# Performance work log

Hardware: AMD Instinct MI355X
Metric: run time of the kernel (lower is better)

Reference implementation:

```python
import jax, jax.numpy as jnp
import numpy as np

B, IN, E, H, MO, OUT, K = 32768, 512, 8, 128, 256, 2, 2


def setup_inputs() -> dict:
    key = jax.random.key(0)
    ks = jax.random.split(key, 9)
    g = lambda k, shape, fan: (jax.random.normal(k, shape, jnp.float32) / np.sqrt(fan)).astype(jnp.float32)
    return {
        "num_prop": jax.random.normal(ks[0], (B, IN), jnp.float32),
        "cat_prop": jax.random.normal(ks[1], (B, 3), jnp.float32),
        "w_gate": g(ks[2], (IN, E), IN),
        "W1": g(ks[3], (E, IN, H), IN),
        "b1": jnp.zeros((E, H), jnp.float32),
        "W2": g(ks[4], (E, H, MO), H),
        "b2": jnp.zeros((E, MO), jnp.float32),
        "Wout": g(ks[5], (MO, OUT), MO),
        "bout": jnp.zeros((OUT,), jnp.float32),
    }


def _cv_squared(v):
    # torch.var is unbiased (ddof=1); eps = 1e-10
    return jnp.var(v, ddof=1) / (jnp.mean(v) ** 2 + 1e-10)


def reference(num_prop, cat_prop, w_gate, W1, b1, W2, b2, Wout, bout):
    b = num_prop.shape[0]
    x = num_prop  # eval mode: dropout is identity, gating noise disabled
    # --- top-k gating ---
    logits = x @ w_gate                                   # [B, E]
    top_vals, top_idx = jax.lax.top_k(logits, K)          # [B, K]
    gate_vals = jax.nn.softmax(top_vals, axis=-1)         # softmax over top-k logits
    gates = jnp.zeros_like(logits).at[jnp.arange(b)[:, None], top_idx].add(gate_vals)  # [B, E]
    # --- load-balancing loss ---
    importance = gates.sum(axis=0)                        # [E]
    load = (gates > 0).astype(jnp.float32).sum(axis=0)    # [E]
    loss = (_cv_squared(importance) + _cv_squared(load)) * 1e-2
    # --- experts (dense-equivalent: gates zero out non-selected experts) ---
    h = jax.nn.relu(jnp.einsum('bi,eih->beh', x, W1) + b1)          # [B, E, H]
    eo = jax.nn.softmax(jnp.einsum('beh,ehm->bem', h, W2) + b2, axis=-1)  # [B, E, MO]
    y = jnp.einsum('be,bem->bm', gates, eo)               # [B, MO]
    # --- output head ---
    out = y @ Wout + bout                                 # [B, OUT]
    return out, loss
```

## Files before the change

### kernel.cpp

```cpp
#include <hip/hip_runtime.h>

#define BN 32768
#define IN 512
#define NE 8
#define NH 128
#define MO 256

typedef const __attribute__((address_space(1))) unsigned int gu32;
typedef __attribute__((address_space(3))) unsigned int lu32;
typedef __attribute__((ext_vector_type(8))) short bf16x8;
typedef __attribute__((ext_vector_type(4))) float f32x4;

__device__ __forceinline__ void cp16(const float* g, float* l) {
    __builtin_amdgcn_global_load_lds((gu32*)g, (lu32*)l, 16, 0, 0);
}

__device__ __forceinline__ unsigned short f2bf(float f) {
    unsigned int u = __float_as_uint(f);
    u = (u + 0x7fffu + ((u >> 16) & 1u)) >> 16;
    return (unsigned short)u;
}
__device__ __forceinline__ float bf2f(unsigned short h) {
    return __uint_as_float((unsigned int)h << 16);
}

__global__ __launch_bounds__(256) void gatep_kernel(
    const float* __restrict__ x, const float* __restrict__ wg,
    const float* __restrict__ W1, const float* __restrict__ W2,
    float* __restrict__ W1F, float* __restrict__ W2F,
    int* __restrict__ gcount, int* __restrict__ gload, float* __restrict__ gimp,
    int* __restrict__ idx_list, float* __restrict__ gate_list,
    float* __restrict__ out, const float* __restrict__ bout)
{
    __shared__ __align__(16) char wb[32768];
    __shared__ int counts_s[NE];
    __shared__ int load_s[NE];
    __shared__ float imp_s[NE];
    __shared__ int base_s[NE];
    __shared__ int rec_e[128];
    __shared__ int rec_p[128];
    __shared__ float rec_g[128];

    int tid = threadIdx.x;
    int bx = blockIdx.x;

    if (bx >= 512) {
        char* pb = wb;
        int t = tid, b = bx - 512;
        if (b < 64) {
            int e = b >> 3, kt = b & 7;
            const float* src = W1 + ((size_t)e * IN + kt * 64) * NH;
            #pragma unroll
            for (int p = 0; p < 8; ++p) {
                int li = p * 256 + t;
                float4 q = *(const float4*)(src + li * 4);
                int kl = li >> 5, n0 = (li & 31) * 4;
                int ks = kl >> 5, g = (kl >> 3) & 3, kb = (kl & 7) * 2;
                float vv[4] = {q.x, q.y, q.z, q.w};
                #pragma unroll
                for (int j = 0; j < 4; ++j) {
                    int n = n0 + j;
                    int off = (((ks * 8 + (n >> 4)) * 64) + (n & 15) + 16 * g) * 16 + kb;
                    unsigned short hh = f2bf(vv[j]);
                    unsigned short hl = f2bf(vv[j] - bf2f(hh));
                    *(unsigned short*)(pb + off) = hh;
                    *(unsigned short*)(pb + 16384 + off) = hl;
                }
            }
            __syncthreads();
            float* dst = W1F + (size_t)b * 8192;
            #pragma unroll
            for (int p = 0; p < 8; ++p) {
                int li = p * 256 + t;
                *(int4*)(dst + li * 4) = *(const int4*)(pb + li * 16);
            }
        } else {
            int bi = b - 64;
            int e = bi >> 2, kt = bi & 3;
            const float* src = W2 + ((size_t)e * NH + kt * 32) * MO;
            #pragma unroll
            for (int p = 0; p < 8; ++p) {
                int li = p * 256 + t;
                float4 q = *(const float4*)(src + li * 4);
                int kl = li >> 6, n0 = (li & 63) * 4;
                int g = kl >> 3, kb = (kl & 7) * 2;
                float vv[4] = {q.x, q.y, q.z, q.w};
                #pragma unroll
                for (int j = 0; j < 4; ++j) {
                    int n = n0 + j;
                    int off = ((n >> 4) * 64 + (n & 15) + 16 * g) * 16 + kb;
                    unsigned short hh = f2bf(vv[j]);
                    unsigned short hl = f2bf(vv[j] - bf2f(hh));
                    *(unsigned short*)(pb + off) = hh;
                    *(unsigned short*)(pb + 16384 + off) = hl;
                }
            }
            __syncthreads();
            float* dst = W2F + (size_t)bi * 8192;
            #pragma unroll
            for (int p = 0; p < 8; ++p) {
                int li = p * 256 + t;
                *(int4*)(dst + li * 4) = *(const int4*)(pb + li * 16);
            }
        }
        return;
    }

    if (tid < NE) { counts_s[tid] = 0; load_s[tid] = 0; imp_s[tid] = 0.f; }
    if (tid < 128) {
        int row = bx * 64 + (tid >> 1);
        out[row * 2 + (tid & 1)] = bout[tid & 1];
    }
    for (int idx = tid; idx < 1024; idx += 256) {
        int ks = idx >> 6, ls = idx & 63;
        int col = ls & 15;
        int kb = 32 * ks + 8 * (ls >> 4);
        unsigned int ph[4], pl[4];
        #pragma unroll
        for (int j = 0; j < 4; ++j) {
            float v0 = (col < 8) ? wg[(kb + 2 * j) * NE + col] : 0.f;
            float v1 = (col < 8) ? wg[(kb + 2 * j + 1) * NE + col] : 0.f;
            unsigned short h0 = f2bf(v0), h1 = f2bf(v1);
            unsigned short l0 = f2bf(v0 - bf2f(h0)), l1 = f2bf(v1 - bf2f(h1));
            ph[j] = (unsigned int)h0 | ((unsigned int)h1 << 16);
            pl[j] = (unsigned int)l0 | ((unsigned int)l1 << 16);
        }
        *(int4*)(wb + ks * 1024 + ls * 16) = make_int4(ph[0], ph[1], ph[2], ph[3]);
        *(int4*)(wb + 16384 + ks * 1024 + ls * 16) = make_int4(pl[0], pl[1], pl[2], pl[3]);
    }
    __syncthreads();

    int w = tid >> 6, l = tid & 63;
    int e = l & 15;
    int rowA = bx * 64 + w * 16 + e;
    const float* px = x + (size_t)rowA * IN + 8 * (l >> 4);

    f32x4 acc = {};
    #pragma unroll
    for (int ks = 0; ks < 16; ++ks) {
        float4 qa = *(const float4*)(px + 32 * ks);
        float4 qb = *(const float4*)(px + 32 * ks + 4);
        float v[8] = {qa.x, qa.y, qa.z, qa.w, qb.x, qb.y, qb.z, qb.w};
        bf16x8 ah, al;
        #pragma unroll
        for (int i = 0; i < 8; ++i) {
            unsigned short h = f2bf(v[i]);
            ah[i] = (short)h;
            al[i] = (short)f2bf(v[i] - bf2f(h));
        }
        bf16x8 bh = *(const bf16x8*)(wb + ks * 1024 + l * 16);
        bf16x8 bl = *(const bf16x8*)(wb + 16384 + ks * 1024 + l * 16);
        acc = __builtin_amdgcn_mfma_f32_16x16x32_bf16(ah, bh, acc, 0, 0, 0);
        acc = __builtin_amdgcn_mfma_f32_16x16x32_bf16(ah, bl, acc, 0, 0, 0);
        acc = __builtin_amdgcn_mfma_f32_16x16x32_bf16(al, bh, acc, 0, 0, 0);
    }

    #pragma unroll
    for (int reg = 0; reg < 4; ++reg) {
        int rloc = w * 16 + 4 * (l >> 4) + reg;
        int row = bx * 64 + rloc;
        float lv = (e < 8) ? acc[reg] : -1e30f;

        float v0 = lv; int e0 = e;
        #pragma unroll
        for (int m = 1; m < 8; m <<= 1) {
            float vo = __shfl_xor(v0, m, 64);
            int eo = __shfl_xor(e0, m, 64);
            if (vo > v0 || (vo == v0 && eo < e0)) { v0 = vo; e0 = eo; }
        }
        float v1 = (e == e0 || e >= 8) ? -1e30f : lv; int e1 = e;
        #pragma unroll
        for (int m = 1; m < 8; m <<= 1) {
            float vo = __shfl_xor(v1, m, 64);
            int eo = __shfl_xor(e1, m, 64);
            if (vo > v1 || (vo == v1 && eo < e1)) { v1 = vo; e1 = eo; }
        }
        float v2 = (e == e0 || e == e1 || e >= 8) ? -1e30f : lv;
        #pragma unroll
        for (int m = 1; m < 8; m <<= 1) v2 = fmaxf(v2, __shfl_xor(v2, m, 64));

        double dv0 = v0, dv1 = v1;
        int f0 = e0, f1 = e1;
        if (e < 8 && v1 - v2 < 2e-4f) {
            const float* xr = x + (size_t)row * IN;
            double d0 = 0, d1 = 0, d2 = 0, d3 = 0;
            for (int k = 0; k < IN; k += 4) {
                float4 xv = *(const float4*)(xr + k);
                d0 = fma((double)xv.x, (double)wg[(k    ) * NE + e], d0);
                d1 = fma((double)xv.y, (double)wg[(k + 1) * NE + e], d1);
                d2 = fma((double)xv.z, (double)wg[(k + 2) * NE + e], d2);
                d3 = fma((double)xv.w, (double)wg[(k + 3) * NE + e], d3);
            }
            double ad = (d0 + d1) + (d2 + d3);
            double w0 = ad; int g0i = e;
            #pragma unroll
            for (int m = 1; m < 8; m <<= 1) {
                double vo = __shfl_xor(w0, m, 64);
                int eo = __shfl_xor(g0i, m, 64);
                if (vo > w0 || (vo == w0 && eo < g0i)) { w0 = vo; g0i = eo; }
            }
            double w1 = (e == g0i) ? -1.0e300 : ad; int g1i = e;
            #pragma unroll
            for (int m = 1; m < 8; m <<= 1) {
                double vo = __shfl_xor(w1, m, 64);
                int eo = __shfl_xor(g1i, m, 64);
                if (vo > w1 || (vo == w1 && eo < g1i)) { w1 = vo; g1i = eo; }
            }
            dv0 = w0; dv1 = w1; f0 = g0i; f1 = g1i;
        }

        if (e == 0) {
            float t1 = expf((float)(dv1 - dv0));
            float s = 1.f + t1;
            float g0 = 1.f / s;
            float g1 = t1 / s;
            atomicAdd(&imp_s[f0], g0);
            atomicAdd(&imp_s[f1], g1);
            if (g0 > 0.f) atomicAdd(&load_s[f0], 1);
            if (g1 > 0.f) atomicAdd(&load_s[f1], 1);
            int p0 = atomicAdd(&counts_s[f0], 1);
            int p1 = atomicAdd(&counts_s[f1], 1);
            int rl = rloc * 2;
            rec_e[rl] = f0; rec_e[rl + 1] = f1;
            rec_g[rl] = g0; rec_g[rl + 1] = g1;
            rec_p[rl] = p0; rec_p[rl + 1] = p1;
        }
    }
    __syncthreads();
    if (tid < NE) {
        base_s[tid] = atomicAdd(&gcount[tid], counts_s[tid]);
        atomicAdd(&gimp[tid], imp_s[tid]);
        atomicAdd(&gload[tid], load_s[tid]);
    }
    __syncthreads();
    if (tid < 128) {
        int ee = rec_e[tid];
        int pos = base_s[ee] + rec_p[tid];
        int rw = bx * 64 + (tid >> 1);
        idx_list[ee * BN + pos] = rw;
        gate_list[ee * BN + pos] = rec_g[tid];
    }
}

__global__ __launch_bounds__(256, 3) void expert_kernel(
    const float* __restrict__ x,
    const float* __restrict__ b1, const float* __restrict__ b2,
    const float* __restrict__ Wout,
    const float* __restrict__ W1F, const float* __restrict__ W2F,
    const int* __restrict__ gcount,
    const float* __restrict__ gimp, const int* __restrict__ gload,
    const int* __restrict__ idx_list, const float* __restrict__ gate_list,
    float* __restrict__ out)
{
    __shared__ __align__(16) char smx[49152];
    __shared__ float woutS[512];

    int e = blockIdx.y;
    int cnt = gcount[e];
    int row0 = blockIdx.x * 64;
    if (e == 0 && blockIdx.x == 0 && threadIdx.x == 0) {
        float mi = 0.f, ml = 0.f;
        for (int k = 0; k < NE; ++k) { mi += gimp[k]; ml += (float)gload[k]; }
        mi *= 0.125f; ml *= 0.125f;
        float vi = 0.f, vl = 0.f;
        for (int k = 0; k < NE; ++k) {
            float d = gimp[k] - mi;  vi += d * d;
            float d2 = (float)gload[k] - ml; vl += d2 * d2;
        }
        vi *= (1.f / 7.f); vl *= (1.f / 7.f);
        out[BN * 2] = (vi / (mi * mi + 1e-10f) + vl / (ml * ml + 1e-10f)) * 0.01f;
    }
    if (row0 >= cnt) return;
    int t = threadIdx.x;
    int l = t & 63, w = t >> 6;

    woutS[t] = Wout[t];
    woutS[256 + t] = Wout[256 + t];

    int s_r  = t & 15;
    int s_g  = (t >> 4) & 3;
    int s_mf = t >> 6;
    int rloc_s = s_mf * 16 + s_r;
    int sgi = row0 + rloc_s; if (sgi >= cnt) sgi = cnt - 1;
    const float* xrow = x + (size_t)idx_list[e * BN + sgi] * IN;

    const float* W1e = W1F + (size_t)e * 65536;
    const float* W2e = W2F + (size_t)e * 32768;

    f32x4 acc1[8] = {};
    for (int kt = 0; kt < 8; ++kt) {
        {
            const float* gb = W1e + (size_t)kt * 8192;
            float* lb = (float*)(smx + 16384);
            #pragma unroll
            for (int p = 0; p < 8; ++p)
                cp16(gb + (p * 256 + t) * 4, lb + (p * 256 + t) * 4);
        }
        #pragma unroll
        for (int ks = 0; ks < 2; ++ks) {
            int k = kt * 64 + ks * 32 + s_g * 8;
            float4 qa = *(const float4*)(xrow + k);
            float4 qb = *(const float4*)(xrow + k + 4);
            float vv[8] = {qa.x, qa.y, qa.z, qa.w, qb.x, qb.y, qb.z, qb.w};
            unsigned int dh[4], dl[4];
            #pragma unroll
            for (int j = 0; j < 4; ++j) {
                unsigned short h0 = f2bf(vv[2 * j]);
                unsigned short h1 = f2bf(vv[2 * j + 1]);
                unsigned short l0 = f2bf(vv[2 * j] - bf2f(h0));
                unsigned short l1 = f2bf(vv[2 * j + 1] - bf2f(h1));
                dh[j] = (unsigned int)h0 | ((unsigned int)h1 << 16);
                dl[j] = (unsigned int)l0 | ((unsigned int)l1 << 16);
            }
            int slot = ((ks * 4 + s_mf) * 64 + (s_r + 16 * s_g)) * 16;
            *(int4*)(smx + slot) = make_int4(dh[0], dh[1], dh[2], dh[3]);
            *(int4*)(smx + 8192 + slot) = make_int4(dl[0], dl[1], dl[2], dl[3]);
        }
        __syncthreads();
        #pragma unroll
        for (int ks = 0; ks < 2; ++ks) {
            int ao = ((ks * 4 + w) * 64 + l) * 16;
            bf16x8 ah = *(const bf16x8*)(smx + ao);
            bf16x8 al = *(const bf16x8*)(smx + 8192 + ao);
            #pragma unroll
            for (int nf = 0; nf < 8; ++nf) {
                int bo = ((ks * 8 + nf) * 64 + l) * 16;
                bf16x8 bh = *(const bf16x8*)(smx + 16384 + bo);
                bf16x8 bl = *(const bf16x8*)(smx + 32768 + bo);
                acc1[nf] = __builtin_amdgcn_mfma_f32_16x16x32_bf16(ah, bh, acc1[nf], 0, 0, 0);
                acc1[nf] = __builtin_amdgcn_mfma_f32_16x16x32_bf16(ah, bl, acc1[nf], 0, 0, 0);
                acc1[nf] = __builtin_amdgcn_mfma_f32_16x16x32_bf16(al, bh, acc1[nf], 0, 0, 0);
                acc1[nf] = __builtin_amdgcn_mfma_f32_16x16x32_bf16(al, bl, acc1[nf], 0, 0, 0);
            }
        }
        __syncthreads();
    }

    {
        int rlow = 4 * (l >> 4);
        #pragma unroll
        for (int nf = 0; nf < 8; ++nf) {
            int c = nf * 16 + (l & 15);
            float b1v = b1[e * NH + c];
            int kt2c = c >> 5;
            int g2 = (c >> 3) & 3;
            int boff = ((kt2c * 4 + w) * 64) * 16 + (c & 7) * 2;
            #pragma unroll
            for (int rg = 0; rg < 4; ++rg) {
                float v = fmaxf(acc1[nf][rg] + b1v, 0.f);
                unsigned short hh = f2bf(v);
                unsigned short hl = f2bf(v - bf2f(hh));
                int off = boff + ((rlow + rg) + 16 * g2) * 16;
                *(unsigned short*)(smx + off) = hh;
                *(unsigned short*)(smx + 16384 + off) = hl;
            }
        }
    }
    __syncthreads();

    f32x4 acc2[16] = {};
    for (int kt2 = 0; kt2 < 4; ++kt2) {
        int ao = ((kt2 * 4 + w) * 64 + l) * 16;
        bf16x8 ah2 = *(const bf16x8*)(smx + ao);
        bf16x8 al2 = *(const bf16x8*)(smx + 16384 + ao);
        #pragma unroll
        for (int nh2 = 0; nh2 < 2; ++nh2) {
            {
                const float* gh = W2e + kt2 * 8192 + nh2 * 2048;
                const float* gl = W2e + kt2 * 8192 + 4096 + nh2 * 2048;
                float* lb = (float*)(smx + 32768);
                #pragma unroll
                for (int p = 0; p < 2; ++p) {
                    cp16(gh + (p * 256 + t) * 4, lb + (p * 256 + t) * 4);
                    cp16(gl + (p * 256 + t) * 4, lb + 2048 + (p * 256 + t) * 4);
                }
            }
            __syncthreads();
            #pragma unroll
            for (int nf2 = 0; nf2 < 8; ++nf2) {
                int bo = (nf2 * 64 + l) * 16;
                bf16x8 bh = *(const bf16x8*)(smx + 32768 + bo);
                bf16x8 bl = *(const bf16x8*)(smx + 40960 + bo);
                int nf = nh2 * 8 + nf2;
                acc2[nf] = __builtin_amdgcn_mfma_f32_16x16x32_bf16(ah2, bh, acc2[nf], 0, 0, 0);
                acc2[nf] = __builtin_amdgcn_mfma_f32_16x16x32_bf16(ah2, bl, acc2[nf], 0, 0, 0);
                acc2[nf] = __builtin_amdgcn_mfma_f32_16x16x32_bf16(al2, bh, acc2[nf], 0, 0, 0);
                acc2[nf] = __builtin_amdgcn_mfma_f32_16x16x32_bf16(al2, bl, acc2[nf], 0, 0, 0);
            }
            __syncthreads();
        }
    }

    #pragma unroll
    for (int nf = 0; nf < 16; ++nf) {
        float b2v = b2[e * MO + nf * 16 + (l & 15)];
        #pragma unroll
        for (int rg = 0; rg < 4; ++rg) acc2[nf][rg] += b2v;
    }
    #pragma unroll
    for (int rg = 0; rg < 4; ++rg) {
        float m = -1e30f;
        #pragma unroll
        for (int nf = 0; nf < 16; ++nf) m = fmaxf(m, acc2[nf][rg]);
        m = fmaxf(m, __shfl_xor(m, 1, 64));
        m = fmaxf(m, __shfl_xor(m, 2, 64));
        m = fmaxf(m, __shfl_xor(m, 4, 64));
        m = fmaxf(m, __shfl_xor(m, 8, 64));
        float s = 0.f, o0 = 0.f, o1 = 0.f;
        #pragma unroll
        for (int nf = 0; nf < 16; ++nf) {
            float tt = __expf(acc2[nf][rg] - m);
            s += tt;
            float2 wv = *(const float2*)&woutS[2 * (nf * 16 + (l & 15))];
            o0 = fmaf(tt, wv.x, o0);
            o1 = fmaf(tt, wv.y, o1);
        }
        s += __shfl_xor(s, 1, 64); s += __shfl_xor(s, 2, 64);
        s += __shfl_xor(s, 4, 64); s += __shfl_xor(s, 8, 64);
        o0 += __shfl_xor(o0, 1, 64); o0 += __shfl_xor(o0, 2, 64);
        o0 += __shfl_xor(o0, 4, 64); o0 += __shfl_xor(o0, 8, 64);
        o1 += __shfl_xor(o1, 1, 64); o1 += __shfl_xor(o1, 2, 64);
        o1 += __shfl_xor(o1, 4, 64); o1 += __shfl_xor(o1, 8, 64);
        if ((l & 15) == 0) {
            int gi = row0 + w * 16 + 4 * (l >> 4) + rg;
            if (gi < cnt) {
                float g = gate_list[e * BN + gi];
                int brow = idx_list[e * BN + gi];
                float inv = 1.f / s;
                atomicAdd(&out[brow * 2 + 0], g * o0 * inv);
                atomicAdd(&out[brow * 2 + 1], g * o1 * inv);
            }
        }
    }
}

extern "C" void kernel_launch(void* const* d_in, const int* in_sizes, int n_in,
                              void* d_out, int out_size, void* d_ws, size_t ws_size,
                              hipStream_t stream) {
    const float* x    = (const float*)d_in[0];
    const float* wg   = (const float*)d_in[2];
    const float* W1   = (const float*)d_in[3];
    const float* b1   = (const float*)d_in[4];
    const float* W2   = (const float*)d_in[5];
    const float* b2   = (const float*)d_in[6];
    const float* Wout = (const float*)d_in[7];
    const float* bout = (const float*)d_in[8];
    float* out = (float*)d_out;

    char* ws = (char*)d_ws;
    int*   gcount    = (int*)(ws + 0);
    int*   gload     = (int*)(ws + 32);
    float* gimp      = (float*)(ws + 64);
    int*   idx_list  = (int*)(ws + 128);
    float* gate_list = (float*)(ws + 128 + sizeof(int) * NE * BN);
    float* W1F       = (float*)(ws + 128 + 8 * NE * BN);
    float* W2F       = (float*)(ws + 128 + 8 * NE * BN + 64 * 32768);

    hipMemsetAsync(ws, 0, 128, stream);
    gatep_kernel<<<608, 256, 0, stream>>>(x, wg, W1, W2, W1F, W2F,
                                          gcount, gload, gimp,
                                          idx_list, gate_list, out, bout);
    dim3 eg(BN / 64, NE);
    expert_kernel<<<eg, 256, 0, stream>>>(x, b1, b2, Wout, W1F, W2F,
                                          gcount, gimp, gload,
                                          idx_list, gate_list, out);
}
```

Measured before the change: 209.0 us.

## Split expert GEMM wave tiling into 2x2 M/N grid with cross-wave softmax reduction

```diff
diff --git a/kernel.cpp b/kernel.cpp
--- a/kernel.cpp
+++ b/kernel.cpp
@@ -253,7 +253,8 @@
     float* __restrict__ out)
 {
     __shared__ __align__(16) char smx[49152];
-    __shared__ float woutS[512];
+    __shared__ float redm[64][2];
+    __shared__ float red3[64][2][3];
 
     int e = blockIdx.y;
     int cnt = gcount[e];
@@ -273,9 +274,8 @@
     if (row0 >= cnt) return;
     int t = threadIdx.x;
     int l = t & 63, w = t >> 6;
-
-    woutS[t] = Wout[t];
-    woutS[256 + t] = Wout[256 + t];
+    int wm = w & 1;
+    int wn = w >> 1;
 
     int s_r  = t & 15;
     int s_g  = (t >> 4) & 3;
@@ -287,7 +287,7 @@
     const float* W1e = W1F + (size_t)e * 65536;
     const float* W2e = W2F + (size_t)e * 32768;
 
-    f32x4 acc1[8] = {};
+    f32x4 acc1[2][4] = {};
     for (int kt = 0; kt < 8; ++kt) {
         {
             const float* gb = W1e + (size_t)kt * 8192;
@@ -319,18 +319,25 @@
         __syncthreads();
         #pragma unroll
         for (int ks = 0; ks < 2; ++ks) {
-            int ao = ((ks * 4 + w) * 64 + l) * 16;
-            bf16x8 ah = *(const bf16x8*)(smx + ao);
-            bf16x8 al = *(const bf16x8*)(smx + 8192 + ao);
-            #pragma unroll
-            for (int nf = 0; nf < 8; ++nf) {
-                int bo = ((ks * 8 + nf) * 64 + l) * 16;
+            bf16x8 ah[2], al[2];
+            #pragma unroll
+            for (int mf = 0; mf < 2; ++mf) {
+                int ao = ((ks * 4 + wm * 2 + mf) * 64 + l) * 16;
+                ah[mf] = *(const bf16x8*)(smx + ao);
+                al[mf] = *(const bf16x8*)(smx + 8192 + ao);
+            }
+            #pragma unroll
+            for (int nfl = 0; nfl < 4; ++nfl) {
+                int bo = ((ks * 8 + wn * 4 + nfl) * 64 + l) * 16;
                 bf16x8 bh = *(const bf16x8*)(smx + 16384 + bo);
                 bf16x8 bl = *(const bf16x8*)(smx + 32768 + bo);
-                acc1[nf] = __builtin_amdgcn_mfma_f32_16x16x32_bf16(ah, bh, acc1[nf], 0, 0, 0);
-                acc1[nf] = __builtin_amdgcn_mfma_f32_16x16x32_bf16(ah, bl, acc1[nf], 0, 0, 0);
-                acc1[nf] = __builtin_amdgcn_mfma_f32_16x16x32_bf16(al, bh, acc1[nf], 0, 0, 0);
-                acc1[nf] = __builtin_amdgcn_mfma_f32_16x16x32_bf16(al, bl, acc1[nf], 0, 0, 0);
+                #pragma unroll
+                for (int mf = 0; mf < 2; ++mf) {
+                    acc1[mf][nfl] = __builtin_amdgcn_mfma_f32_16x16x32_bf16(ah[mf], bh, acc1[mf][nfl], 0, 0, 0);
+                    acc1[mf][nfl] = __builtin_amdgcn_mfma_f32_16x16x32_bf16(ah[mf], bl, acc1[mf][nfl], 0, 0, 0);
+                    acc1[mf][nfl] = __builtin_amdgcn_mfma_f32_16x16x32_bf16(al[mf], bh, acc1[mf][nfl], 0, 0, 0);
+                    acc1[mf][nfl] = __builtin_amdgcn_mfma_f32_16x16x32_bf16(al[mf], bl, acc1[mf][nfl], 0, 0, 0);
+                }
             }
         }
         __syncthreads();
@@ -339,35 +346,43 @@
     {
         int rlow = 4 * (l >> 4);
         #pragma unroll
-        for (int nf = 0; nf < 8; ++nf) {
-            int c = nf * 16 + (l & 15);
-            float b1v = b1[e * NH + c];
-            int kt2c = c >> 5;
-            int g2 = (c >> 3) & 3;
-            int boff = ((kt2c * 4 + w) * 64) * 16 + (c & 7) * 2;
-            #pragma unroll
-            for (int rg = 0; rg < 4; ++rg) {
-                float v = fmaxf(acc1[nf][rg] + b1v, 0.f);
-                unsigned short hh = f2bf(v);
-                unsigned short hl = f2bf(v - bf2f(hh));
-                int off = boff + ((rlow + rg) + 16 * g2) * 16;
-                *(unsigned short*)(smx + off) = hh;
-                *(unsigned short*)(smx + 16384 + off) = hl;
+        for (int mf = 0; mf < 2; ++mf) {
+            int mf2 = wm * 2 + mf;
+            #pragma unroll
+            for (int nfl = 0; nfl < 4; ++nfl) {
+                int c = wn * 64 + nfl * 16 + (l & 15);
+                float b1v = b1[e * NH + c];
+                int kt2c = c >> 5;
+                int g2 = (c >> 3) & 3;
+                int boff = ((kt2c * 4 + mf2) * 64) * 16 + (c & 7) * 2;
+                #pragma unroll
+                for (int rg = 0; rg < 4; ++rg) {
+                    float v = fmaxf(acc1[mf][nfl][rg] + b1v, 0.f);
+                    unsigned short hh = f2bf(v);
+                    unsigned short hl = f2bf(v - bf2f(hh));
+                    int off = boff + ((rlow + rg) + 16 * g2) * 16;
+                    *(unsigned short*)(smx + off) = hh;
+                    *(unsigned short*)(smx + 16384 + off) = hl;
+                }
             }
         }
     }
     __syncthreads();
 
-    f32x4 acc2[16] = {};
+    f32x4 acc2[2][8] = {};
     for (int kt2 = 0; kt2 < 4; ++kt2) {
-        int ao = ((kt2 * 4 + w) * 64 + l) * 16;
-        bf16x8 ah2 = *(const bf16x8*)(smx + ao);
-        bf16x8 al2 = *(const bf16x8*)(smx + 16384 + ao);
-        #pragma unroll
-        for (int nh2 = 0; nh2 < 2; ++nh2) {
+        bf16x8 ah2[2], al2[2];
+        #pragma unroll
+        for (int mf = 0; mf < 2; ++mf) {
+            int ao = ((kt2 * 4 + wm * 2 + mf) * 64 + l) * 16;
+            ah2[mf] = *(const bf16x8*)(smx + ao);
+            al2[mf] = *(const bf16x8*)(smx + 16384 + ao);
+        }
+        #pragma unroll
+        for (int ch = 0; ch < 2; ++ch) {
             {
-                const float* gh = W2e + kt2 * 8192 + nh2 * 2048;
-                const float* gl = W2e + kt2 * 8192 + 4096 + nh2 * 2048;
+                const float* gh = W2e + kt2 * 8192 + ch * 2048;
+                const float* gl = W2e + kt2 * 8192 + 4096 + ch * 2048;
                 float* lb = (float*)(smx + 32768);
                 #pragma unroll
                 for (int p = 0; p < 2; ++p) {
@@ -377,60 +392,95 @@
             }
             __syncthreads();
             #pragma unroll
-            for (int nf2 = 0; nf2 < 8; ++nf2) {
-                int bo = (nf2 * 64 + l) * 16;
+            for (int nf2 = 0; nf2 < 4; ++nf2) {
+                int bo = ((wn * 4 + nf2) * 64 + l) * 16;
                 bf16x8 bh = *(const bf16x8*)(smx + 32768 + bo);
                 bf16x8 bl = *(const bf16x8*)(smx + 40960 + bo);
-                int nf = nh2 * 8 + nf2;
-                acc2[nf] = __builtin_amdgcn_mfma_f32_16x16x32_bf16(ah2, bh, acc2[nf], 0, 0, 0);
-                acc2[nf] = __builtin_amdgcn_mfma_f32_16x16x32_bf16(ah2, bl, acc2[nf], 0, 0, 0);
-                acc2[nf] = __builtin_amdgcn_mfma_f32_16x16x32_bf16(al2, bh, acc2[nf], 0, 0, 0);
-                acc2[nf] = __builtin_amdgcn_mfma_f32_16x16x32_bf16(al2, bl, acc2[nf], 0, 0, 0);
+                int nf = ch * 4 + nf2;
+                #pragma unroll
+                for (int mf = 0; mf < 2; ++mf) {
+                    acc2[mf][nf] = __builtin_amdgcn_mfma_f32_16x16x32_bf16(ah2[mf], bh, acc2[mf][nf], 0, 0, 0);
+                    acc2[mf][nf] = __builtin_amdgcn_mfma_f32_16x16x32_bf16(ah2[mf], bl, acc2[mf][nf], 0, 0, 0);
+                    acc2[mf][nf] = __builtin_amdgcn_mfma_f32_16x16x32_bf16(al2[mf], bh, acc2[mf][nf], 0, 0, 0);
+                    acc2[mf][nf] = __builtin_amdgcn_mfma_f32_16x16x32_bf16(al2[mf], bl, acc2[mf][nf], 0, 0, 0);
+                }
             }
             __syncthreads();
         }
     }
 
+    float2 wrow[8];
     #pragma unroll
-    for (int nf = 0; nf < 16; ++nf) {
-        float b2v = b2[e * MO + nf * 16 + (l & 15)];
-        #pragma unroll
-        for (int rg = 0; rg < 4; ++rg) acc2[nf][rg] += b2v;
+    for (int nf = 0; nf < 8; ++nf) {
+        int c = (nf >> 2) * 128 + (wn * 4 + (nf & 3)) * 16 + (l & 15);
+        float b2v = b2[e * MO + c];
+        #pragma unroll
+        for (int rg = 0; rg < 4; ++rg) {
+            acc2[0][nf][rg] += b2v;
+            acc2[1][nf][rg] += b2v;
+        }
+        wrow[nf] = *(const float2*)&Wout[2 * c];
     }
     #pragma unroll
-    for (int rg = 0; rg < 4; ++rg) {
-        float m = -1e30f;
-        #pragma unroll
-        for (int nf = 0; nf < 16; ++nf) m = fmaxf(m, acc2[nf][rg]);
-        m = fmaxf(m, __shfl_xor(m, 1, 64));
-        m = fmaxf(m, __shfl_xor(m, 2, 64));
-        m = fmaxf(m, __shfl_xor(m, 4, 64));
-        m = fmaxf(m, __shfl_xor(m, 8, 64));
-        float s = 0.f, o0 = 0.f, o1 = 0.f;
-        #pragma unroll
-        for (int nf = 0; nf < 16; ++nf) {
-            float tt = __expf(acc2[nf][rg] - m);
-            s += tt;
-            float2 wv = *(const float2*)&woutS[2 * (nf * 16 + (l & 15))];
-            o0 = fmaf(tt, wv.x, o0);
-            o1 = fmaf(tt, wv.y, o1);
-        }
-        s += __shfl_xor(s, 1, 64); s += __shfl_xor(s, 2, 64);
-        s += __shfl_xor(s, 4, 64); s += __shfl_xor(s, 8, 64);
-        o0 += __shfl_xor(o0, 1, 64); o0 += __shfl_xor(o0, 2, 64);
-        o0 += __shfl_xor(o0, 4, 64); o0 += __shfl_xor(o0, 8, 64);
-        o1 += __shfl_xor(o1, 1, 64); o1 += __shfl_xor(o1, 2, 64);
-        o1 += __shfl_xor(o1, 4, 64); o1 += __shfl_xor(o1, 8, 64);
-        if ((l & 15) == 0) {
-            int gi = row0 + w * 16 + 4 * (l >> 4) + rg;
-            if (gi < cnt) {
-                float g = gate_list[e * BN + gi];
-                int brow = idx_list[e * BN + gi];
-                float inv = 1.f / s;
-                atomicAdd(&out[brow * 2 + 0], g * o0 * inv);
-                atomicAdd(&out[brow * 2 + 1], g * o1 * inv);
-            }
-        }
+    for (int mf = 0; mf < 2; ++mf)
+        #pragma unroll
+        for (int rg = 0; rg < 4; ++rg) {
+            float m = -1e30f;
+            #pragma unroll
+            for (int nf = 0; nf < 8; ++nf) m = fmaxf(m, acc2[mf][nf][rg]);
+            m = fmaxf(m, __shfl_xor(m, 1, 64));
+            m = fmaxf(m, __shfl_xor(m, 2, 64));
+            m = fmaxf(m, __shfl_xor(m, 4, 64));
+            m = fmaxf(m, __shfl_xor(m, 8, 64));
+            int rloc = wm * 32 + mf * 16 + 4 * (l >> 4) + rg;
+            if ((l & 15) == 0) redm[rloc][wn] = m;
+        }
+    __syncthreads();
+    #pragma unroll
+    for (int mf = 0; mf < 2; ++mf)
+        #pragma unroll
+        for (int rg = 0; rg < 4; ++rg) {
+            int rloc = wm * 32 + mf * 16 + 4 * (l >> 4) + rg;
+            float M = fmaxf(redm[rloc][0], redm[rloc][1]);
+            float s = 0.f, o0 = 0.f, o1 = 0.f;
+            #pragma unroll
+            for (int nf = 0; nf < 8; ++nf) {
+                float tt = __expf(acc2[mf][nf][rg] - M);
+                s += tt;
+                o0 = fmaf(tt, wrow[nf].x, o0);
+                o1 = fmaf(tt, wrow[nf].y, o1);
+            }
+            s += __shfl_xor(s, 1, 64); s += __shfl_xor(s, 2, 64);
+            s += __shfl_xor(s, 4, 64); s += __shfl_xor(s, 8, 64);
+            o0 += __shfl_xor(o0, 1, 64); o0 += __shfl_xor(o0, 2, 64);
+            o0 += __shfl_xor(o0, 4, 64); o0 += __shfl_xor(o0, 8, 64);
+            o1 += __shfl_xor(o1, 1, 64); o1 += __shfl_xor(o1, 2, 64);
+            o1 += __shfl_xor(o1, 4, 64); o1 += __shfl_xor(o1, 8, 64);
+            if ((l & 15) == 0) {
+                red3[rloc][wn][0] = s;
+                red3[rloc][wn][1] = o0;
+                red3[rloc][wn][2] = o1;
+            }
+        }
+    __syncthreads();
+    if (wn == 0 && (l & 15) == 0) {
+        #pragma unroll
+        for (int mf = 0; mf < 2; ++mf)
+            #pragma unroll
+            for (int rg = 0; rg < 4; ++rg) {
+                int rloc = wm * 32 + mf * 16 + 4 * (l >> 4) + rg;
+                float S  = red3[rloc][0][0] + red3[rloc][1][0];
+                float O0 = red3[rloc][0][1] + red3[rloc][1][1];
+                float O1 = red3[rloc][0][2] + red3[rloc][1][2];
+                int gi = row0 + rloc;
+                if (gi < cnt) {
+                    float g = gate_list[e * BN + gi];
+                    int brow = idx_list[e * BN + gi];
+                    float inv = 1.f / S;
+                    atomicAdd(&out[brow * 2 + 0], g * O0 * inv);
+                    atomicAdd(&out[brow * 2 + 1], g * O1 * inv);
+                }
+            }
     }
 }
 
```

Result: no change. 211.1 us (+1.0%).

## Double-buffer W1/W2 LDS tiles and load x fragments directly to registers

Applied to the files above, without the earlier changes.

```diff
diff --git a/kernel.cpp b/kernel.cpp
--- a/kernel.cpp
+++ b/kernel.cpp
@@ -242,7 +242,7 @@
     }
 }
 
-__global__ __launch_bounds__(256, 3) void expert_kernel(
+__global__ __launch_bounds__(256, 2) void expert_kernel(
     const float* __restrict__ x,
     const float* __restrict__ b1, const float* __restrict__ b2,
     const float* __restrict__ Wout,
@@ -252,8 +252,7 @@
     const int* __restrict__ idx_list, const float* __restrict__ gate_list,
     float* __restrict__ out)
 {
-    __shared__ __align__(16) char smx[49152];
-    __shared__ float woutS[512];
+    __shared__ __align__(16) char smx[65536];
 
     int e = blockIdx.y;
     int cnt = gcount[e];
@@ -274,74 +273,98 @@
     int t = threadIdx.x;
     int l = t & 63, w = t >> 6;
 
-    woutS[t] = Wout[t];
-    woutS[256 + t] = Wout[256 + t];
-
-    int s_r  = t & 15;
-    int s_g  = (t >> 4) & 3;
-    int s_mf = t >> 6;
-    int rloc_s = s_mf * 16 + s_r;
-    int sgi = row0 + rloc_s; if (sgi >= cnt) sgi = cnt - 1;
-    const float* xrow = x + (size_t)idx_list[e * BN + sgi] * IN;
+    int rA = row0 + w * 16 + (l & 15);
+    if (rA >= cnt) rA = cnt - 1;
+    const float* pA = x + (size_t)idx_list[e * BN + rA] * IN + 8 * (l >> 4);
+
+    float b1r[8];
+    #pragma unroll
+    for (int nf = 0; nf < 8; ++nf) b1r[nf] = b1[e * NH + nf * 16 + (l & 15)];
 
     const float* W1e = W1F + (size_t)e * 65536;
     const float* W2e = W2F + (size_t)e * 32768;
 
+    float4 rx[2][2];
+    rx[0][0] = *(const float4*)(pA);
+    rx[0][1] = *(const float4*)(pA + 4);
+    rx[1][0] = *(const float4*)(pA + 32);
+    rx[1][1] = *(const float4*)(pA + 36);
+    {
+        float* lb = (float*)smx;
+        #pragma unroll
+        for (int p = 0; p < 8; ++p)
+            cp16(W1e + (p * 256 + t) * 4, lb + (p * 256 + t) * 4);
+    }
+
     f32x4 acc1[8] = {};
+    #pragma unroll
     for (int kt = 0; kt < 8; ++kt) {
-        {
-            const float* gb = W1e + (size_t)kt * 8192;
-            float* lb = (float*)(smx + 16384);
+        float4 rn[2][2];
+        if (kt < 7) {
+            const float* pn = pA + (kt + 1) * 64;
+            rn[0][0] = *(const float4*)(pn);
+            rn[0][1] = *(const float4*)(pn + 4);
+            rn[1][0] = *(const float4*)(pn + 32);
+            rn[1][1] = *(const float4*)(pn + 36);
+            const float* gb = W1e + (size_t)(kt + 1) * 8192;
+            float* lb = (float*)(smx + ((kt + 1) & 1) * 32768);
             #pragma unroll
             for (int p = 0; p < 8; ++p)
                 cp16(gb + (p * 256 + t) * 4, lb + (p * 256 + t) * 4);
         }
+        __builtin_amdgcn_sched_barrier(0);
+        bf16x8 ah[2], al[2];
         #pragma unroll
         for (int ks = 0; ks < 2; ++ks) {
-            int k = kt * 64 + ks * 32 + s_g * 8;
-            float4 qa = *(const float4*)(xrow + k);
-            float4 qb = *(const float4*)(xrow + k + 4);
-            float vv[8] = {qa.x, qa.y, qa.z, qa.w, qb.x, qb.y, qb.z, qb.w};
-            unsigned int dh[4], dl[4];
-            #pragma unroll
-            for (int j = 0; j < 4; ++j) {
-                unsigned short h0 = f2bf(vv[2 * j]);
-                unsigned short h1 = f2bf(vv[2 * j + 1]);
-                unsigned short l0 = f2bf(vv[2 * j] - bf2f(h0));
-                unsigned short l1 = f2bf(vv[2 * j + 1] - bf2f(h1));
-                dh[j] = (unsigned int)h0 | ((unsigned int)h1 << 16);
-                dl[j] = (unsigned int)l0 | ((unsigned int)l1 << 16);
-            }
-            int slot = ((ks * 4 + s_mf) * 64 + (s_r + 16 * s_g)) * 16;
-            *(int4*)(smx + slot) = make_int4(dh[0], dh[1], dh[2], dh[3]);
-            *(int4*)(smx + 8192 + slot) = make_int4(dl[0], dl[1], dl[2], dl[3]);
-        }
-        __syncthreads();
-        #pragma unroll
-        for (int ks = 0; ks < 2; ++ks) {
-            int ao = ((ks * 4 + w) * 64 + l) * 16;
-            bf16x8 ah = *(const bf16x8*)(smx + ao);
-            bf16x8 al = *(const bf16x8*)(smx + 8192 + ao);
+            float v[8] = {rx[ks][0].x, rx[ks][0].y, rx[ks][0].z, rx[ks][0].w,
+                          rx[ks][1].x, rx[ks][1].y, rx[ks][1].z, rx[ks][1].w};
+            #pragma unroll
+            for (int i = 0; i < 8; ++i) {
+                unsigned short h = f2bf(v[i]);
+                ah[ks][i] = (short)h;
+                al[ks][i] = (short)f2bf(v[i] - bf2f(h));
+            }
+        }
+        if (kt < 7) asm volatile("s_waitcnt vmcnt(12)" ::: "memory");
+        else        asm volatile("s_waitcnt vmcnt(0)" ::: "memory");
+        __builtin_amdgcn_sched_barrier(0);
+        __builtin_amdgcn_s_barrier();
+        __builtin_amdgcn_sched_barrier(0);
+        const char* wbase = smx + (kt & 1) * 32768;
+        #pragma unroll
+        for (int ks = 0; ks < 2; ++ks)
             #pragma unroll
             for (int nf = 0; nf < 8; ++nf) {
                 int bo = ((ks * 8 + nf) * 64 + l) * 16;
-                bf16x8 bh = *(const bf16x8*)(smx + 16384 + bo);
-                bf16x8 bl = *(const bf16x8*)(smx + 32768 + bo);
-                acc1[nf] = __builtin_amdgcn_mfma_f32_16x16x32_bf16(ah, bh, acc1[nf], 0, 0, 0);
-                acc1[nf] = __builtin_amdgcn_mfma_f32_16x16x32_bf16(ah, bl, acc1[nf], 0, 0, 0);
-                acc1[nf] = __builtin_amdgcn_mfma_f32_16x16x32_bf16(al, bh, acc1[nf], 0, 0, 0);
-                acc1[nf] = __builtin_amdgcn_mfma_f32_16x16x32_bf16(al, bl, acc1[nf], 0, 0, 0);
-            }
-        }
-        __syncthreads();
-    }
-
+                bf16x8 bh = *(const bf16x8*)(wbase + bo);
+                bf16x8 bl = *(const bf16x8*)(wbase + 16384 + bo);
+                acc1[nf] = __builtin_amdgcn_mfma_f32_16x16x32_bf16(ah[ks], bh, acc1[nf], 0, 0, 0);
+                acc1[nf] = __builtin_amdgcn_mfma_f32_16x16x32_bf16(ah[ks], bl, acc1[nf], 0, 0, 0);
+                acc1[nf] = __builtin_amdgcn_mfma_f32_16x16x32_bf16(al[ks], bh, acc1[nf], 0, 0, 0);
+                acc1[nf] = __builtin_amdgcn_mfma_f32_16x16x32_bf16(al[ks], bl, acc1[nf], 0, 0, 0);
+            }
+        __builtin_amdgcn_sched_barrier(0);
+        __builtin_amdgcn_s_barrier();
+        if (kt < 7) {
+            rx[0][0] = rn[0][0]; rx[0][1] = rn[0][1];
+            rx[1][0] = rn[1][0]; rx[1][1] = rn[1][1];
+        }
+    }
+
+    {
+        float* lb = (float*)(smx + 32768);
+        #pragma unroll
+        for (int p = 0; p < 2; ++p) {
+            cp16(W2e + (p * 256 + t) * 4, lb + (p * 256 + t) * 4);
+            cp16(W2e + 4096 + (p * 256 + t) * 4, lb + 2048 + (p * 256 + t) * 4);
+        }
+    }
     {
         int rlow = 4 * (l >> 4);
         #pragma unroll
         for (int nf = 0; nf < 8; ++nf) {
             int c = nf * 16 + (l & 15);
-            float b1v = b1[e * NH + c];
+            float b1v = b1r[nf];
             int kt2c = c >> 5;
             int g2 = (c >> 3) & 3;
             int boff = ((kt2c * 4 + w) * 64) * 16 + (c & 7) * 2;
@@ -356,39 +379,50 @@
             }
         }
     }
-    __syncthreads();
+    asm volatile("s_waitcnt lgkmcnt(0)" ::: "memory");
+    __builtin_amdgcn_sched_barrier(0);
 
     f32x4 acc2[16] = {};
-    for (int kt2 = 0; kt2 < 4; ++kt2) {
-        int ao = ((kt2 * 4 + w) * 64 + l) * 16;
-        bf16x8 ah2 = *(const bf16x8*)(smx + ao);
-        bf16x8 al2 = *(const bf16x8*)(smx + 16384 + ao);
-        #pragma unroll
-        for (int nh2 = 0; nh2 < 2; ++nh2) {
-            {
-                const float* gh = W2e + kt2 * 8192 + nh2 * 2048;
-                const float* gl = W2e + kt2 * 8192 + 4096 + nh2 * 2048;
-                float* lb = (float*)(smx + 32768);
-                #pragma unroll
-                for (int p = 0; p < 2; ++p) {
-                    cp16(gh + (p * 256 + t) * 4, lb + (p * 256 + t) * 4);
-                    cp16(gl + (p * 256 + t) * 4, lb + 2048 + (p * 256 + t) * 4);
-                }
-            }
-            __syncthreads();
-            #pragma unroll
-            for (int nf2 = 0; nf2 < 8; ++nf2) {
-                int bo = (nf2 * 64 + l) * 16;
-                bf16x8 bh = *(const bf16x8*)(smx + 32768 + bo);
-                bf16x8 bl = *(const bf16x8*)(smx + 40960 + bo);
-                int nf = nh2 * 8 + nf2;
-                acc2[nf] = __builtin_amdgcn_mfma_f32_16x16x32_bf16(ah2, bh, acc2[nf], 0, 0, 0);
-                acc2[nf] = __builtin_amdgcn_mfma_f32_16x16x32_bf16(ah2, bl, acc2[nf], 0, 0, 0);
-                acc2[nf] = __builtin_amdgcn_mfma_f32_16x16x32_bf16(al2, bh, acc2[nf], 0, 0, 0);
-                acc2[nf] = __builtin_amdgcn_mfma_f32_16x16x32_bf16(al2, bl, acc2[nf], 0, 0, 0);
-            }
-            __syncthreads();
-        }
+    bf16x8 ah2 = {}, al2 = {};
+    #pragma unroll
+    for (int c = 0; c < 8; ++c) {
+        int kt2 = c >> 1, nh2 = c & 1;
+        if (c < 7) {
+            int kn = c + 1;
+            const float* gh = W2e + (kn >> 1) * 8192 + (kn & 1) * 2048;
+            const float* gl = gh + 4096;
+            float* lb = (float*)(smx + 32768 + (kn & 1) * 16384);
+            #pragma unroll
+            for (int p = 0; p < 2; ++p) {
+                cp16(gh + (p * 256 + t) * 4, lb + (p * 256 + t) * 4);
+                cp16(gl + (p * 256 + t) * 4, lb + 2048 + (p * 256 + t) * 4);
+            }
+        }
+        __builtin_amdgcn_sched_barrier(0);
+        if ((c & 1) == 0) {
+            int ao = ((kt2 * 4 + w) * 64 + l) * 16;
+            ah2 = *(const bf16x8*)(smx + ao);
+            al2 = *(const bf16x8*)(smx + 16384 + ao);
+        }
+        if (c < 7) asm volatile("s_waitcnt vmcnt(4)" ::: "memory");
+        else       asm volatile("s_waitcnt vmcnt(0)" ::: "memory");
+        __builtin_amdgcn_sched_barrier(0);
+        __builtin_amdgcn_s_barrier();
+        __builtin_amdgcn_sched_barrier(0);
+        const char* cb = smx + 32768 + (c & 1) * 16384;
+        #pragma unroll
+        for (int nf2 = 0; nf2 < 8; ++nf2) {
+            int bo = (nf2 * 64 + l) * 16;
+            bf16x8 bh = *(const bf16x8*)(cb + bo);
+            bf16x8 bl = *(const bf16x8*)(cb + 8192 + bo);
+            int nf = nh2 * 8 + nf2;
+            acc2[nf] = __builtin_amdgcn_mfma_f32_16x16x32_bf16(ah2, bh, acc2[nf], 0, 0, 0);
+            acc2[nf] = __builtin_amdgcn_mfma_f32_16x16x32_bf16(ah2, bl, acc2[nf], 0, 0, 0);
+            acc2[nf] = __builtin_amdgcn_mfma_f32_16x16x32_bf16(al2, bh, acc2[nf], 0, 0, 0);
+            acc2[nf] = __builtin_amdgcn_mfma_f32_16x16x32_bf16(al2, bl, acc2[nf], 0, 0, 0);
+        }
+        __builtin_amdgcn_sched_barrier(0);
+        __builtin_amdgcn_s_barrier();
     }
 
     #pragma unroll
@@ -411,7 +445,7 @@
         for (int nf = 0; nf < 16; ++nf) {
             float tt = __expf(acc2[nf][rg] - m);
             s += tt;
-            float2 wv = *(const float2*)&woutS[2 * (nf * 16 + (l & 15))];
+            float2 wv = *(const float2*)&Wout[2 * (nf * 16 + (l & 15))];
             o0 = fmaf(tt, wv.x, o0);
             o1 = fmaf(tt, wv.y, o1);
         }
```

Result: slower. 213.4 us (+2.1%).
